# Performance work log

Measured on AMD Instinct MI355X. Metric: run time of the kernel, lower is better.

The kernel has to match this reference:

```python
import jax, jax.numpy as jnp
import numpy as np

# 8 neighbor offsets (dy, dx) in unfold row-major order with center (0,0) removed
NEIGHBOR_OFFSETS = [(-1, -1), (-1, 0), (-1, 1), (0, -1), (0, 1), (1, -1), (1, 0), (1, 1)]


def setup_inputs() -> dict:
    key = jax.random.key(0)
    B, H, W, L, C = 8, 16, 16, 64, 64
    E_flat = jax.random.normal(key, (B, H * W, L, C), dtype=jnp.float32)
    return {"E_flat": E_flat, "H": H, "W": W}


def reference(E_flat, H, W):
    B, P, L, C = E_flat.shape
    assert P == H * W
    # restore grid: [B, H, W, L, C]
    E_grid = E_flat.reshape(B, H, W, L, C)
    # zero-pad spatial dims by 1 (matches nn.Unfold padding=1)
    pad = jnp.pad(E_grid, ((0, 0), (1, 1), (1, 1), (0, 0), (0, 0)))
    # gather 8 shifted views; stack on new axis after L -> [B, H, W, L, 8, C]
    neigh = jnp.stack(
        [pad[:, 1 + dy:1 + dy + H, 1 + dx:1 + dx + W] for dy, dx in NEIGHBOR_OFFSETS],
        axis=4,
    )
    # [B, patches, length*8, input_size]
    return neigh.reshape(B, H * W, L * 8, C)
```

## Files before the change

### kernel.cpp

```cpp
#include <hip/hip_runtime.h>


constexpr unsigned Bb = 8, Hh = 16, Ww = 16, Ll = 64, Cc = 64;
constexpr unsigned C4   = Cc / 4;
constexpr unsigned OUT4 = Bb * Hh * Ww * Ll * 8u * C4;

__global__ __launch_bounds__(256) void patch_neighbor_gather(
    const float4* __restrict__ in, float4* __restrict__ out) {
  unsigned i = blockIdx.x * blockDim.x + threadIdx.x;
  const unsigned stride = gridDim.x * blockDim.x;
  const float4 zero = make_float4(0.f, 0.f, 0.f, 0.f);
  for (; i < OUT4; i += stride) {
    const unsigned c4 = i & 15u;
    const unsigned n  = (i >> 4) & 7u;
    const unsigned l  = (i >> 7) & 63u;
    const unsigned p  = (i >> 13) & 255u;
    const unsigned b  = i >> 21;
    const int h = (int)(p >> 4);
    const int w = (int)(p & 15u);
    const int dy = (int)((0xA940u >> (2u * n)) & 3u) - 1;
    const int dx = (int)((0x9224u >> (2u * n)) & 3u) - 1;
    const int hh = h + dy;
    const int ww = w + dx;
    float4 v = zero;
    if ((unsigned)hh < Hh && (unsigned)ww < Ww) {
      const unsigned src = (b << 18) | ((unsigned)hh << 14) |
                           ((unsigned)ww << 10) | (l << 4) | c4;
      v = in[src];
    }
    out[i] = v;
  }
}

extern "C" void kernel_launch(void* const* d_in, const int* in_sizes, int n_in,
                              void* d_out, int out_size, void* d_ws, size_t ws_size,
                              hipStream_t stream) {
  const float4* in = (const float4*)d_in[0];
  float4* out = (float4*)d_out;
  const int threads = 256;
  const int blocks  = 2048;
  patch_neighbor_gather<<<blocks, threads, 0, stream>>>(in, out);
}
```

Baseline: 309.4 us.

## Replace output-indexed gather with input-indexed scatter using nontemporal accesses

The kernel now has one thread per input float4. Each thread loads its element once and writes it to every neighbor slot that references it, and it also writes zeros into its own out-of-bounds neighbor slots. This removes the repeated reads of each input element and the grid-stride loop, and the nontemporal hints are meant to keep streaming data from polluting the cache. The cost is scattered stores and divergent branches within a wave, which may lower store coalescing across the output.

```diff
diff --git a/kernel.cpp b/kernel.cpp
--- a/kernel.cpp
+++ b/kernel.cpp
@@ -1,43 +1,49 @@
 #include <hip/hip_runtime.h>
 
 
-constexpr unsigned Bb = 8, Hh = 16, Ww = 16, Ll = 64, Cc = 64;
-constexpr unsigned C4   = Cc / 4;
-constexpr unsigned OUT4 = Bb * Hh * Ww * Ll * 8u * C4;
+typedef float f32x4 __attribute__((ext_vector_type(4)));
 
-__global__ __launch_bounds__(256) void patch_neighbor_gather(
-    const float4* __restrict__ in, float4* __restrict__ out) {
-  unsigned i = blockIdx.x * blockDim.x + threadIdx.x;
-  const unsigned stride = gridDim.x * blockDim.x;
-  const float4 zero = make_float4(0.f, 0.f, 0.f, 0.f);
-  for (; i < OUT4; i += stride) {
-    const unsigned c4 = i & 15u;
-    const unsigned n  = (i >> 4) & 7u;
-    const unsigned l  = (i >> 7) & 63u;
-    const unsigned p  = (i >> 13) & 255u;
-    const unsigned b  = i >> 21;
-    const int h = (int)(p >> 4);
-    const int w = (int)(p & 15u);
-    const int dy = (int)((0xA940u >> (2u * n)) & 3u) - 1;
-    const int dx = (int)((0x9224u >> (2u * n)) & 3u) - 1;
-    const int hh = h + dy;
-    const int ww = w + dx;
-    float4 v = zero;
-    if ((unsigned)hh < Hh && (unsigned)ww < Ww) {
-      const unsigned src = (b << 18) | ((unsigned)hh << 14) |
-                           ((unsigned)ww << 10) | (l << 4) | c4;
-      v = in[src];
+constexpr unsigned IN4 = 8u * 256u * 64u * 16u;
+
+__global__ __launch_bounds__(256) void patch_scatter(
+    const f32x4* __restrict__ in, f32x4* __restrict__ out) {
+  const unsigned i = blockIdx.x * 256u + threadIdx.x;
+  const unsigned c4 = i & 15u;
+  const unsigned l  = (i >> 4) & 63u;
+  const unsigned p  = (i >> 10) & 255u;
+  const unsigned b  = i >> 18;
+  const int h = (int)(p >> 4);
+  const int w = (int)(p & 15u);
+
+  const f32x4 v = __builtin_nontemporal_load(&in[i]);
+  const f32x4 z = {0.f, 0.f, 0.f, 0.f};
+
+  const unsigned obase = (b << 21) | (l << 7) | c4;
+  const unsigned zbase = obase | (p << 13);
+
+  constexpr int DY[8] = {-1, -1, -1,  0, 0,  1, 1, 1};
+  constexpr int DX[8] = {-1,  0,  1, -1, 1, -1, 0, 1};
+#pragma unroll
+  for (int n = 0; n < 8; ++n) {
+    const int hh = h - DY[n];
+    const int ww = w - DX[n];
+    if (((unsigned)hh < 16u) & ((unsigned)ww < 16u)) {
+      const unsigned dst =
+          obase | ((unsigned)((hh << 4) | ww) << 13) | ((unsigned)n << 4);
+      __builtin_nontemporal_store(v, &out[dst]);
     }
-    out[i] = v;
+    const int h2 = h + DY[n];
+    const int w2 = w + DX[n];
+    if (!(((unsigned)h2 < 16u) & ((unsigned)w2 < 16u))) {
+      __builtin_nontemporal_store(z, &out[zbase | ((unsigned)n << 4)]);
+    }
   }
 }
 
 extern "C" void kernel_launch(void* const* d_in, const int* in_sizes, int n_in,
                               void* d_out, int out_size, void* d_ws, size_t ws_size,
                               hipStream_t stream) {
-  const float4* in = (const float4*)d_in[0];
-  float4* out = (float4*)d_out;
-  const int threads = 256;
-  const int blocks  = 2048;
-  patch_neighbor_gather<<<blocks, threads, 0, stream>>>(in, out);
+  const f32x4* in = (const f32x4*)d_in[0];
+  f32x4* out = (f32x4*)d_out;
+  patch_scatter<<<IN4 / 256u, 256, 0, stream>>>(in, out);
 }
```

Measured after the change: 283.5 us. 8.4% less time.
